# Kernel tuning notes

Hardware: AMD Instinct MI355X
Metric: run time of the kernel (lower is better)

Reference implementation:

```python
import jax, jax.numpy as jnp
import numpy as np

# Model dims
T0 = 2048      # tokens (batch*seq flattened)
D = 2048       # hidden_size
E = 256        # n_routed_experts
K = 8          # num_experts_per_tok
G = 8          # expert groups
EG = 32        # experts per group
R = 64         # tucker rank
I = 1408       # moe_intermediate_size


def setup_inputs() -> dict:
    key = jax.random.key(0)
    ks = jax.random.split(key, 12)
    f = lambda k, s: jax.random.normal(k, s, dtype=jnp.float32) * 0.02
    return {
        "hidden_states": jax.random.normal(ks[0], (T0, D), dtype=jnp.float32),
        "w_gate": f(ks[1], (D, E)),
        # Tucker factors per group: shared in-factor A, per-expert core C, shared out-factor B
        "A_gate": f(ks[2], (G, D, R)), "C_gate": f(ks[3], (G, EG, R, R)), "B_gate": f(ks[4], (G, R, I)),
        "A_up":   f(ks[5], (G, D, R)), "C_up":   f(ks[6], (G, EG, R, R)), "B_up":   f(ks[7], (G, R, I)),
        "A_down": f(ks[8], (G, I, R)), "C_down": f(ks[9], (G, EG, R, R)), "B_down": f(ks[10], (G, R, D)),
    }


def _tucker(x, A, C, B, inner):
    # x: [T, d_in], A: [d_in, R], C: [EG, R, R] gathered per-token, B: [R, d_out]
    h1 = x @ A                                    # [T, R]
    h2 = jnp.einsum('tr,trs->ts', h1, C[inner])   # per-token expert core
    return h2 @ B                                 # [T, d_out]


def reference(hidden_states, w_gate, A_gate, C_gate, B_gate,
              A_up, C_up, B_up, A_down, C_down, B_down):
    # Router: softmax in fp32, top-k, renormalize
    logits = hidden_states @ w_gate                              # [T0, E]
    probs = jax.nn.softmax(logits.astype(jnp.float32), axis=-1)
    rw, sel = jax.lax.top_k(probs, K)                            # [T0, K]
    rw = (rw / rw.sum(axis=-1, keepdims=True)).astype(hidden_states.dtype)

    idx = sel.reshape(-1)          # [T0*K] expert ids of dispatched rows
    gid = idx // EG                # group id
    inner = idx % EG               # expert within group
    x = jnp.repeat(hidden_states, K, axis=0)   # repeat_interleave dispatch [T0*K, D]

    out = jnp.zeros_like(x)
    for g in range(G):             # static loop over 8 structurally distinct groups
        m = (gid == g)[:, None]
        xg = jnp.where(m, x, 0.0)  # masked dispatch (zeros flow to zero through the MLP)
        go = _tucker(xg, A_gate[g], C_gate[g], B_gate[g], inner)
        uo = _tucker(xg, A_up[g],   C_up[g],   B_up[g],   inner)
        inter = jax.nn.silu(go) * uo
        do = _tucker(inter, A_down[g], C_down[g], B_down[g], inner)
        out = out + jnp.where(m, do, 0.0)

    # weighted combine
    return (out.reshape(T0, K, D) * rw[..., None]).sum(axis=1)
```

## Files before the change

### kernel.cpp

```cpp
#include <hip/hip_runtime.h>
#include <math.h>

constexpr int T0n = 2048;
constexpr int Dn  = 2048;
constexpr int En  = 256;
constexpr int Gn  = 8;
constexpr int EGn = 32;
constexpr int Rn  = 64;
constexpr int In  = 1408;

constexpr int NROWS = T0n * 8;
constexpr int SEGCAP = NROWS;
constexpr int KS_R = 4;
constexpr int NTILE_MAX = NROWS / 128 + Gn;
constexpr int CSPLIT = 8;

typedef __attribute__((ext_vector_type(8))) short s8v;
typedef __attribute__((ext_vector_type(4))) float f4v;
typedef __attribute__((ext_vector_type(4))) int i4v;
#define MFMA16(a, b, c) __builtin_amdgcn_mfma_f32_16x16x32_bf16(a, b, c, 0, 0, 0)
#define MFMAI8(a, b, c) __builtin_amdgcn_mfma_i32_16x16x64_i8(a, b, c, 0, 0, 0)

__device__ __forceinline__ unsigned short f2bf(float x) {
  unsigned int u = __float_as_uint(x);
  unsigned int r = (u + 0x7FFFu + ((u >> 16) & 1u)) >> 16;
  return (unsigned short)r;
}

struct TD { const float* src; unsigned short* dst; int rows, cols, nbx, per_batch, base; };
struct TD9 { TD t[9]; };

__global__ __launch_bounds__(256) void k_tcvt9(TD9 D) {
  __shared__ float tbuf[32][33];
  int id = blockIdx.x;
  int ti = 0;
#pragma unroll
  for (int i = 1; i < 9; ++i) ti = (id >= D.t[i].base) ? i : ti;
  TD d = D.t[ti];
  int local = id - d.base;
  int bz = local / d.per_batch;
  int rem = local - bz * d.per_batch;
  int by = rem / d.nbx;
  int bx = rem - by * d.nbx;

  size_t boff = (size_t)bz * d.rows * d.cols;
  const float* src = d.src + boff;
  unsigned short* dst = d.dst + boff;
  int c0 = bx * 32, r0 = by * 32;
  int tx = threadIdx.x & 31, ty = threadIdx.x >> 5;
  for (int i = ty; i < 32; i += 8)
    tbuf[i][tx] = src[(size_t)(r0 + i) * d.cols + c0 + tx];
  __syncthreads();
  for (int i = ty; i < 32; i += 8)
    dst[(size_t)(c0 + i) * d.rows + r0 + tx] = f2bf(tbuf[tx][i]);
}

__device__ __forceinline__ int4 limbs4(float v, double sc) {
  double d = (double)v * sc;
  d = fmin(fmax(d, -2.0e9), 2.0e9);
  int x = __double2int_rn(d);
  int l0 = (int)(signed char)(x & 0xff); x = (x - l0) >> 8;
  int l1 = (int)(signed char)(x & 0xff); x = (x - l1) >> 8;
  int l2 = (int)(signed char)(x & 0xff); x = (x - l2) >> 8;
  return make_int4(l0, l1, l2, x);
}

__global__ __launch_bounds__(256) void k_quant_h(
    const float* __restrict__ H, char* __restrict__ hq) {
  const size_t PL = (size_t)T0n * Dn;
  size_t i = (size_t)blockIdx.x * 256 + threadIdx.x;
  float4 v = *(const float4*)&H[i * 4];
  int4 a = limbs4(v.x, 268435456.0);
  int4 b = limbs4(v.y, 268435456.0);
  int4 c = limbs4(v.z, 268435456.0);
  int4 d = limbs4(v.w, 268435456.0);
  unsigned int p0 = (a.x & 0xff) | ((b.x & 0xff) << 8) | ((c.x & 0xff) << 16) | ((unsigned)(d.x & 0xff) << 24);
  unsigned int p1 = (a.y & 0xff) | ((b.y & 0xff) << 8) | ((c.y & 0xff) << 16) | ((unsigned)(d.y & 0xff) << 24);
  unsigned int p2 = (a.z & 0xff) | ((b.z & 0xff) << 8) | ((c.z & 0xff) << 16) | ((unsigned)(d.z & 0xff) << 24);
  unsigned int p3 = (a.w & 0xff) | ((b.w & 0xff) << 8) | ((c.w & 0xff) << 16) | ((unsigned)(d.w & 0xff) << 24);
  *(unsigned int*)&hq[0 * PL + i * 4] = p0;
  *(unsigned int*)&hq[1 * PL + i * 4] = p1;
  *(unsigned int*)&hq[2 * PL + i * 4] = p2;
  *(unsigned int*)&hq[3 * PL + i * 4] = p3;
}

__global__ __launch_bounds__(256) void k_quant_wT(
    const float* __restrict__ W, char* __restrict__ wqT) {
  __shared__ float tb[32][33];
  const size_t PL = (size_t)En * Dn;
  int kb = blockIdx.x * 32, nb = blockIdx.y * 32;
  int tx = threadIdx.x & 31, ty = threadIdx.x >> 5;
  for (int i = ty; i < 32; i += 8)
    tb[i][tx] = W[(size_t)(kb + i) * En + nb + tx];
  __syncthreads();
  for (int i = ty; i < 32; i += 8) {
    int4 l = limbs4(tb[tx][i], 8589934592.0);
    size_t off = (size_t)(nb + i) * Dn + kb + tx;
    wqT[0 * PL + off] = (char)l.x;
    wqT[1 * PL + off] = (char)l.y;
    wqT[2 * PL + off] = (char)l.z;
    wqT[3 * PL + off] = (char)l.w;
  }
}

__global__ __launch_bounds__(256) void k_router_i8(
    const char* __restrict__ hq, const char* __restrict__ wqT,
    float* __restrict__ part) {
  __shared__ __align__(16) char Asl[4][64][80];
  __shared__ __align__(16) char Bsl[4][64][80];
  const int n0 = blockIdx.x * 64, m0 = blockIdx.y * 64;
  const int kc = blockIdx.z;
  const int tid = threadIdx.x;
  const int w = tid >> 6, ln = tid & 63;
  const int quad = ln >> 4, lane16 = ln & 15;

  const char* ha = hq + ((size_t)w * T0n + m0 + ln) * Dn;
  const char* ba = wqT + ((size_t)w * En + n0 + ln) * Dn;

  i4v acc[4][5] = {};

  const int kbeg = kc * (Dn / KS_R);
  for (int k0 = kbeg; k0 < kbeg + Dn / KS_R; k0 += 64) {
#pragma unroll
    for (int q = 0; q < 4; ++q) {
      *(uint4*)&Asl[w][ln][q * 16] = *(const uint4*)&ha[k0 + q * 16];
      *(uint4*)&Bsl[w][ln][q * 16] = *(const uint4*)&ba[k0 + q * 16];
    }
    __syncthreads();
    i4v b0 = *(const i4v*)&Bsl[0][w * 16 + lane16][quad * 16];
    i4v b1 = *(const i4v*)&Bsl[1][w * 16 + lane16][quad * 16];
    i4v b2 = *(const i4v*)&Bsl[2][w * 16 + lane16][quad * 16];
    i4v b3 = *(const i4v*)&Bsl[3][w * 16 + lane16][quad * 16];
#pragma unroll
    for (int mt = 0; mt < 4; ++mt) {
      i4v a0 = *(const i4v*)&Asl[0][mt * 16 + lane16][quad * 16];
      i4v a1 = *(const i4v*)&Asl[1][mt * 16 + lane16][quad * 16];
      i4v a2 = *(const i4v*)&Asl[2][mt * 16 + lane16][quad * 16];
      i4v a3 = *(const i4v*)&Asl[3][mt * 16 + lane16][quad * 16];
      acc[mt][0] = MFMAI8(a0, b2, acc[mt][0]);
      acc[mt][0] = MFMAI8(a1, b1, acc[mt][0]);
      acc[mt][0] = MFMAI8(a2, b0, acc[mt][0]);
      acc[mt][1] = MFMAI8(a0, b3, acc[mt][1]);
      acc[mt][1] = MFMAI8(a1, b2, acc[mt][1]);
      acc[mt][1] = MFMAI8(a2, b1, acc[mt][1]);
      acc[mt][1] = MFMAI8(a3, b0, acc[mt][1]);
      acc[mt][2] = MFMAI8(a1, b3, acc[mt][2]);
      acc[mt][2] = MFMAI8(a2, b2, acc[mt][2]);
      acc[mt][2] = MFMAI8(a3, b1, acc[mt][2]);
      acc[mt][3] = MFMAI8(a2, b3, acc[mt][3]);
      acc[mt][3] = MFMAI8(a3, b2, acc[mt][3]);
      acc[mt][4] = MFMAI8(a3, b3, acc[mt][4]);
    }
    __syncthreads();
  }

  float* prow = part + (size_t)kc * T0n * En;
#pragma unroll
  for (int mt = 0; mt < 4; ++mt)
#pragma unroll
    for (int r = 0; r < 4; ++r) {
      int row = m0 + mt * 16 + quad * 4 + r;
      int col = n0 + w * 16 + lane16;
      double v = (double)acc[mt][0][r] * 0x1p-45 +
                 (double)acc[mt][1][r] * 0x1p-37 +
                 (double)acc[mt][2][r] * 0x1p-29 +
                 (double)acc[mt][3][r] * 0x1p-21 +
                 (double)acc[mt][4][r] * 0x1p-13;
      prow[(size_t)row * En + col] = (float)v;
    }
}

__global__ __launch_bounds__(256) void k_topk(
    const float* __restrict__ part, int* __restrict__ sel,
    float* __restrict__ rw, int* __restrict__ cnt_e) {
  const int wid = threadIdx.x >> 6, ln = threadIdx.x & 63;
  const int t = blockIdx.x * 4 + wid;

  double v[4];
#pragma unroll
  for (int j = 0; j < 4; ++j) {
    double s = 0.0;
#pragma unroll
    for (int kc = 0; kc < KS_R; ++kc)
      s += (double)part[((size_t)kc * T0n + t) * En + ln + 64 * j];
    v[j] = s;
  }

  float topv[8];
  int topi[8];
#pragma unroll
  for (int k = 0; k < 8; ++k) {
    double bv = v[0]; int bi = ln;
#pragma unroll
    for (int j = 1; j < 4; ++j) {
      int cand = ln + 64 * j;
      if (v[j] > bv || (v[j] == bv && cand < bi)) { bv = v[j]; bi = cand; }
    }
#pragma unroll
    for (int off = 32; off > 0; off >>= 1) {
      double ov = __shfl_xor(bv, off);
      int oi = __shfl_xor(bi, off);
      if (ov > bv || (ov == bv && oi < bi)) { bv = ov; bi = oi; }
    }
    topv[k] = (float)bv; topi[k] = bi;
    if ((bi & 63) == ln) v[bi >> 6] = -1e300;
  }

  if (ln < 8) {
    float m = topv[0];
    float ssum = 0.f;
#pragma unroll
    for (int k = 0; k < 8; ++k) ssum += expf(topv[k] - m);
    rw[t * 8 + ln] = expf(topv[ln] - m) / ssum;
    sel[t * 8 + ln] = topi[ln];
    atomicAdd(&cnt_e[topi[ln]], 1);
  }
}

__global__ __launch_bounds__(256) void k_scan(
    const int* __restrict__ cnt_e, int* __restrict__ off_e,
    int* __restrict__ cur_e, int* __restrict__ grp_n) {
  __shared__ int c[256];
  int tid = threadIdx.x;
  c[tid] = cnt_e[tid];
  __syncthreads();
  int g = tid >> 5, ei = tid & 31;
  int run = 0;
  for (int i = 0; i < ei; ++i) run += c[(g << 5) + i];
  off_e[tid] = g * SEGCAP + run;
  cur_e[tid] = g * SEGCAP + run;
  if (ei == 31) grp_n[g] = run + c[tid];
}

__global__ void k_scatter(const int* __restrict__ sel, int* __restrict__ cur_e,
                          int* __restrict__ rseg) {
  int i = blockIdx.x * 256 + threadIdx.x;
  int e = sel[i];
  int pos = atomicAdd(&cur_e[e], 1);
  rseg[pos] = i;
}

__global__ __launch_bounds__(512) void k_h1_mfma(
    const float* __restrict__ H,
    const unsigned short* __restrict__ AgT, const unsigned short* __restrict__ AuT,
    unsigned short* __restrict__ h1gb, unsigned short* __restrict__ h1ub) {
  const int t0 = blockIdx.x * 64;
  const int g = blockIdx.y;
  const unsigned short* Wg = AgT + (size_t)g * Rn * Dn;
  const unsigned short* Wu = AuT + (size_t)g * Rn * Dn;

  __shared__ unsigned short As[64 * 72];
  __shared__ unsigned short Bg_l[64 * 72];
  __shared__ unsigned short Bu_l[64 * 72];
  const int tid = threadIdx.x;
  const int w = tid >> 6, ln = tid & 63;
  const int path = w >> 2, ws = w & 3;
  const int quad = ln >> 4, lane16 = ln & 15;
  const int j = tid >> 3, q = (tid & 7) * 8;

  f4v S[4] = {};

  for (int k0 = 0; k0 < Dn; k0 += 64) {
    {
      float4 v0 = *(const float4*)&H[(size_t)(t0 + j) * Dn + k0 + q];
      float4 v1 = *(const float4*)&H[(size_t)(t0 + j) * Dn + k0 + q + 4];
      ushort4 o0, o1;
      o0.x = f2bf(v0.x); o0.y = f2bf(v0.y); o0.z = f2bf(v0.z); o0.w = f2bf(v0.w);
      o1.x = f2bf(v1.x); o1.y = f2bf(v1.y); o1.z = f2bf(v1.z); o1.w = f2bf(v1.w);
      *(ushort4*)&As[j * 72 + q] = o0;
      *(ushort4*)&As[j * 72 + q + 4] = o1;
      *(uint4*)&Bg_l[j * 72 + q] = *(const uint4*)&Wg[(size_t)j * Dn + k0 + q];
      *(uint4*)&Bu_l[j * 72 + q] = *(const uint4*)&Wu[(size_t)j * Dn + k0 + q];
    }
    __syncthreads();
    const unsigned short* Bl = path ? Bu_l : Bg_l;
#pragma unroll
    for (int kk = 0; kk < 2; ++kk) {
      s8v a = *(const s8v*)&As[(ws * 16 + lane16) * 72 + kk * 32 + quad * 8];
#pragma unroll
      for (int nt = 0; nt < 4; ++nt) {
        s8v b = *(const s8v*)&Bl[(nt * 16 + lane16) * 72 + kk * 32 + quad * 8];
        S[nt] = MFMA16(a, b, S[nt]);
      }
    }
    __syncthreads();
  }
  unsigned short* out = path ? h1ub : h1gb;
#pragma unroll
  for (int nt = 0; nt < 4; ++nt)
#pragma unroll
    for (int r = 0; r < 4; ++r) {
      int row = t0 + ws * 16 + quad * 4 + r;
      int col = g * 64 + nt * 16 + lane16;
      out[(size_t)row * (Gn * Rn) + col] = f2bf(S[nt][r]);
    }
}

__global__ __launch_bounds__(512) void k_core_gu(
    const unsigned short* __restrict__ h1gb, const unsigned short* __restrict__ h1ub,
    const unsigned short* __restrict__ CgT, const unsigned short* __restrict__ CuT,
    const int* __restrict__ rseg, const int* __restrict__ off_e,
    const int* __restrict__ cnt_e,
    unsigned short* __restrict__ h2gb, unsigned short* __restrict__ h2ub) {
  const int e = blockIdx.x;
  const int ne = cnt_e[e];
  if (ne == 0) return;
  const int g = e >> 5;
  const int base = off_e[e];
  __shared__ unsigned short Cg_l[64 * 72];
  __shared__ unsigned short Cu_l[64 * 72];
  __shared__ unsigned short Ags[64 * 72];
  __shared__ unsigned short Aus[64 * 72];
  __shared__ int rids[64];
  const int tid = threadIdx.x;
  const int w = tid >> 6, ln = tid & 63;
  const int path = w >> 2, ws = w & 3;
  const int quad = ln >> 4, lane16 = ln & 15;
  const int j = tid >> 3, q = (tid & 7) * 8;
  {
    const unsigned short* cg = CgT + (size_t)e * (Rn * Rn);
    const unsigned short* cu = CuT + (size_t)e * (Rn * Rn);
    *(uint4*)&Cg_l[j * 72 + q] = *(const uint4*)&cg[j * 64 + q];
    *(uint4*)&Cu_l[j * 72 + q] = *(const uint4*)&cu[j * 64 + q];
  }
  const int ntile = (ne + 63) >> 6;
  for (int it = 0; it < ntile; ++it) {
    int mi = it * 64 + j;
    int rid = (mi < ne) ? rseg[base + mi] : -1;
    if ((tid & 7) == 0) rids[j] = rid;
    uint4 zg = {0, 0, 0, 0}, zu = {0, 0, 0, 0};
    if (rid >= 0) {
      zg = *(const uint4*)&h1gb[(size_t)(rid >> 3) * (Gn * Rn) + g * 64 + q];
      zu = *(const uint4*)&h1ub[(size_t)(rid >> 3) * (Gn * Rn) + g * 64 + q];
    }
    *(uint4*)&Ags[j * 72 + q] = zg;
    *(uint4*)&Aus[j * 72 + q] = zu;
    __syncthreads();
    const unsigned short* Al = path ? Aus : Ags;
    const unsigned short* Cl = path ? Cu_l : Cg_l;
    f4v S[4] = {};
#pragma unroll
    for (int kk = 0; kk < 2; ++kk) {
      s8v a = *(const s8v*)&Al[(ws * 16 + lane16) * 72 + kk * 32 + quad * 8];
#pragma unroll
      for (int nt = 0; nt < 4; ++nt) {
        s8v b = *(const s8v*)&Cl[(nt * 16 + lane16) * 72 + kk * 32 + quad * 8];
        S[nt] = MFMA16(a, b, S[nt]);
      }
    }
    unsigned short* out = path ? h2ub : h2gb;
#pragma unroll
    for (int nt = 0; nt < 4; ++nt)
#pragma unroll
      for (int r = 0; r < 4; ++r) {
        int rid2 = rids[ws * 16 + quad * 4 + r];
        if (rid2 >= 0)
          out[(size_t)rid2 * 64 + nt * 16 + lane16] = f2bf(S[nt][r]);
      }
    __syncthreads();
  }
}

__global__ __launch_bounds__(256) void k_expand_mfma(
    const unsigned short* __restrict__ h2gb, const unsigned short* __restrict__ h2ub,
    const unsigned short* __restrict__ BgT, const unsigned short* __restrict__ BuT,
    const unsigned short* __restrict__ AdT,
    const int* __restrict__ rseg, const int* __restrict__ grp_n,
    float* __restrict__ h1d) {
  int t = blockIdx.x;
  int g = -1, m0 = 0, ng = 0;
  {
    int pre = 0;
#pragma unroll
    for (int gg = 0; gg < Gn; ++gg) {
      int n = grp_n[gg];
      int nt = (n + 127) >> 7;
      if (g < 0 && t < pre + nt) { g = gg; m0 = (t - pre) << 7; ng = n; }
      pre += nt;
    }
  }
  if (g < 0) return;
  const int c_beg = (blockIdx.y * 22) / CSPLIT;
  const int c_end = ((blockIdx.y + 1) * 22) / CSPLIT;

  __shared__ unsigned short Bg_l[64 * 72];
  __shared__ unsigned short Bu_l[64 * 72];
  __shared__ unsigned short Ad_l[64 * 72];
  __shared__ unsigned short inter_l[4][32 * 72];
  __shared__ int rids[128];

  const int tid = threadIdx.x;
  const int w = tid >> 6, ln = tid & 63;
  const int quad = ln >> 4, lane16 = ln & 15;

  if (tid < 128) rids[tid] = (m0 + tid < ng) ? rseg[g * SEGCAP + m0 + tid] : -1;
  __syncthreads();

  s8v ag[2][2], au[2][2];
#pragma unroll
  for (int mt = 0; mt < 2; ++mt) {
    int rid = rids[w * 32 + mt * 16 + lane16];
#pragma unroll
    for (int kk = 0; kk < 2; ++kk) {
      s8v zg = {}, zu = {};
      if (rid >= 0) {
        zg = *(const s8v*)&h2gb[(size_t)rid * 64 + kk * 32 + quad * 8];
        zu = *(const s8v*)&h2ub[(size_t)rid * 64 + kk * 32 + quad * 8];
      }
      ag[mt][kk] = zg;
      au[mt][kk] = zu;
    }
  }

  const unsigned short* Bg_base = BgT + (size_t)g * In * Rn;
  const unsigned short* Bu_base = BuT + (size_t)g * In * Rn;
  const unsigned short* Ad_base = AdT + (size_t)g * Rn * In;

  unsigned short* ib = &inter_l[w][0];
  f4v P[2][4] = {};

  for (int c = c_beg; c < c_end; ++c) {
    const int i0 = c * 64;
#pragma unroll
    for (int i = 0; i < 2; ++i) {
      int cq = tid + i * 256;
      int row = cq >> 3, co = (cq & 7) * 8;
      *(uint4*)&Bg_l[row * 72 + co] = *(const uint4*)&Bg_base[(size_t)(i0 + row) * Rn + co];
      *(uint4*)&Bu_l[row * 72 + co] = *(const uint4*)&Bu_base[(size_t)(i0 + row) * Rn + co];
      *(uint4*)&Ad_l[row * 72 + co] = *(const uint4*)&Ad_base[(size_t)row * In + i0 + co];
    }
    __syncthreads();

    f4v Sg[2][4] = {}, Su[2][4] = {};
#pragma unroll
    for (int kk = 0; kk < 2; ++kk) {
      s8v bg[4], bu[4];
#pragma unroll
      for (int nt = 0; nt < 4; ++nt) {
        bg[nt] = *(const s8v*)&Bg_l[(nt * 16 + lane16) * 72 + kk * 32 + quad * 8];
        bu[nt] = *(const s8v*)&Bu_l[(nt * 16 + lane16) * 72 + kk * 32 + quad * 8];
      }
#pragma unroll
      for (int mt = 0; mt < 2; ++mt)
#pragma unroll
        for (int nt = 0; nt < 4; ++nt) {
          Sg[mt][nt] = MFMA16(ag[mt][kk], bg[nt], Sg[mt][nt]);
          Su[mt][nt] = MFMA16(au[mt][kk], bu[nt], Su[mt][nt]);
        }
    }

#pragma unroll
    for (int mt = 0; mt < 2; ++mt)
#pragma unroll
      for (int nt = 0; nt < 4; ++nt)
#pragma unroll
        for (int r = 0; r < 4; ++r) {
          float sg = Sg[mt][nt][r];
          float v = sg / (1.f + __expf(-sg)) * Su[mt][nt][r];
          ib[(mt * 16 + quad * 4 + r) * 72 + nt * 16 + lane16] = f2bf(v);
        }
    asm volatile("s_waitcnt lgkmcnt(0)" ::: "memory");

#pragma unroll
    for (int kk = 0; kk < 2; ++kk) {
      s8v ai[2], bd[4];
#pragma unroll
      for (int mt = 0; mt < 2; ++mt)
        ai[mt] = *(const s8v*)&ib[(mt * 16 + lane16) * 72 + kk * 32 + quad * 8];
#pragma unroll
      for (int nt = 0; nt < 4; ++nt)
        bd[nt] = *(const s8v*)&Ad_l[(nt * 16 + lane16) * 72 + kk * 32 + quad * 8];
#pragma unroll
      for (int mt = 0; mt < 2; ++mt)
#pragma unroll
        for (int nt = 0; nt < 4; ++nt)
          P[mt][nt] = MFMA16(ai[mt], bd[nt], P[mt][nt]);
    }
    __syncthreads();
  }

#pragma unroll
  for (int mt = 0; mt < 2; ++mt)
#pragma unroll
    for (int nt = 0; nt < 4; ++nt)
#pragma unroll
      for (int r = 0; r < 4; ++r) {
        int lrow = w * 32 + mt * 16 + quad * 4 + r;
        int rid = rids[lrow];
        if (rid >= 0)
          atomicAdd(&h1d[(size_t)rid * 64 + nt * 16 + lane16], P[mt][nt][r]);
      }
}

__global__ __launch_bounds__(512) void k_core_down(
    const float* __restrict__ h1d, const unsigned short* __restrict__ CdT,
    const float* __restrict__ rw,
    const int* __restrict__ rseg, const int* __restrict__ off_e,
    const int* __restrict__ cnt_e,
    float* __restrict__ y) {
  const int e = blockIdx.x;
  const int ne = cnt_e[e];
  if (ne == 0) return;
  const int g = e >> 5;
  const int base = off_e[e];
  __shared__ unsigned short Bd_l[64 * 72];
  __shared__ unsigned short Ad_l[128 * 72];
  __shared__ int rids[128];
  const int tid = threadIdx.x;
  const int w = tid >> 6, ln = tid & 63;
  const int quad = ln >> 4, lane16 = ln & 15;
  {
    int j = tid >> 3, q = (tid & 7) * 8;
    const unsigned short* cd = CdT + (size_t)e * (Rn * Rn);
    *(uint4*)&Bd_l[j * 72 + q] = *(const uint4*)&cd[j * 64 + q];
  }
  const int gj = tid >> 2, gq = (tid & 3) * 16;
  const int ntile = (ne + 127) >> 7;
  for (int it = 0; it < ntile; ++it) {
    int mi = it * 128 + gj;
    int rid = (mi < ne) ? rseg[base + mi] : -1;
    if ((tid & 3) == 0) rids[gj] = rid;
#pragma unroll
    for (int i = 0; i < 4; ++i) {
      int kb = gq + i * 4;
      float4 vd = {0.f, 0.f, 0.f, 0.f};
      if (rid >= 0) vd = *(const float4*)&h1d[(size_t)rid * 64 + kb];
      ushort4 od;
      od.x = f2bf(vd.x); od.y = f2bf(vd.y); od.z = f2bf(vd.z); od.w = f2bf(vd.w);
      *(ushort4*)&Ad_l[gj * 72 + kb] = od;
    }
    __syncthreads();
    f4v Sd[4] = {};
#pragma unroll
    for (int kk = 0; kk < 2; ++kk) {
      s8v ad = *(const s8v*)&Ad_l[(w * 16 + lane16) * 72 + kk * 32 + quad * 8];
#pragma unroll
      for (int nt = 0; nt < 4; ++nt) {
        s8v bd = *(const s8v*)&Bd_l[(nt * 16 + lane16) * 72 + kk * 32 + quad * 8];
        Sd[nt] = MFMA16(ad, bd, Sd[nt]);
      }
    }
#pragma unroll
    for (int nt = 0; nt < 4; ++nt)
#pragma unroll
      for (int r = 0; r < 4; ++r) {
        int rid2 = rids[w * 16 + quad * 4 + r];
        if (rid2 >= 0) {
          float wgt = rw[rid2];
          atomicAdd(&y[(size_t)(rid2 >> 3) * (Gn * Rn) + g * 64 + nt * 16 + lane16],
                    wgt * Sd[nt][r]);
        }
      }
    __syncthreads();
  }
}

__global__ __launch_bounds__(256) void k_combine(
    const float* __restrict__ y, const unsigned short* __restrict__ BdT,
    float* __restrict__ outp) {
  const int t0 = blockIdx.y * 128, n0 = blockIdx.x * 128;
  __shared__ unsigned short As[128 * 72];
  __shared__ unsigned short Bs[128 * 72];
  const int tid = threadIdx.x;
  const int w = tid >> 6, ln = tid & 63;
  const int quad = ln >> 4, lane16 = ln & 15;
  const int mbase = (w >> 1) * 64, nbase = (w & 1) * 64;

  f4v acc[4][4] = {};

  for (int k0 = 0; k0 < Gn * Rn; k0 += 64) {
#pragma unroll
    for (int i = 0; i < 8; ++i) {
      int c = tid + i * 256;
      int row = c >> 4, cc = (c & 15) * 4;
      float4 v = *(const float4*)&y[(size_t)(t0 + row) * (Gn * Rn) + k0 + cc];
      ushort4 o;
      o.x = f2bf(v.x); o.y = f2bf(v.y); o.z = f2bf(v.z); o.w = f2bf(v.w);
      *(ushort4*)&As[row * 72 + cc] = o;
    }
#pragma unroll
    for (int i = 0; i < 4; ++i) {
      int c = tid + i * 256;
      int row = c >> 3, cc = (c & 7) * 8;
      *(uint4*)&Bs[row * 72 + cc] = *(const uint4*)&BdT[(size_t)(n0 + row) * (Gn * Rn) + k0 + cc];
    }
    __syncthreads();
#pragma unroll
    for (int kk = 0; kk < 2; ++kk) {
      s8v a[4], b[4];
#pragma unroll
      for (int mt = 0; mt < 4; ++mt)
        a[mt] = *(const s8v*)&As[(mbase + mt * 16 + lane16) * 72 + kk * 32 + quad * 8];
#pragma unroll
      for (int nt = 0; nt < 4; ++nt)
        b[nt] = *(const s8v*)&Bs[(nbase + nt * 16 + lane16) * 72 + kk * 32 + quad * 8];
#pragma unroll
      for (int mt = 0; mt < 4; ++mt)
#pragma unroll
        for (int nt = 0; nt < 4; ++nt)
          acc[mt][nt] = MFMA16(a[mt], b[nt], acc[mt][nt]);
    }
    __syncthreads();
  }
#pragma unroll
  for (int mt = 0; mt < 4; ++mt)
#pragma unroll
    for (int nt = 0; nt < 4; ++nt)
#pragma unroll
      for (int r = 0; r < 4; ++r)
        outp[(size_t)(t0 + mbase + mt * 16 + quad * 4 + r) * Dn +
             n0 + nbase + nt * 16 + lane16] = acc[mt][nt][r];
}

extern "C" void kernel_launch(void* const* d_in, const int* in_sizes, int n_in,
                              void* d_out, int out_size, void* d_ws, size_t ws_size,
                              hipStream_t stream) {
  const float* hidden = (const float*)d_in[0];
  const float* w_gate = (const float*)d_in[1];
  const float* A_gate = (const float*)d_in[2];
  const float* C_gate = (const float*)d_in[3];
  const float* B_gate = (const float*)d_in[4];
  const float* A_up   = (const float*)d_in[5];
  const float* C_up   = (const float*)d_in[6];
  const float* B_up   = (const float*)d_in[7];
  const float* A_down = (const float*)d_in[8];
  const float* C_down = (const float*)d_in[9];
  const float* B_down = (const float*)d_in[10];
  float* out = (float*)d_out;

  char* base = (char*)d_ws;
  size_t o = 0;
  unsigned short* h2gb = (unsigned short*)(base + o); o += (size_t)NROWS * Rn * 2;
  unsigned short* h2ub = (unsigned short*)(base + o); o += (size_t)NROWS * Rn * 2;
  unsigned short* AgT  = (unsigned short*)(base + o); o += (size_t)Gn * Rn * Dn * 2;
  unsigned short* AuT  = (unsigned short*)(base + o); o += (size_t)Gn * Rn * Dn * 2;
  unsigned short* BgT  = (unsigned short*)(base + o); o += (size_t)Gn * In * Rn * 2;
  unsigned short* BuT  = (unsigned short*)(base + o); o += (size_t)Gn * In * Rn * 2;
  unsigned short* AdT  = (unsigned short*)(base + o); o += (size_t)Gn * Rn * In * 2;
  unsigned short* BdT  = (unsigned short*)(base + o); o += (size_t)Dn * Gn * Rn * 2;
  unsigned short* CgT  = (unsigned short*)(base + o); o += (size_t)En * Rn * Rn * 2;
  unsigned short* CuT  = (unsigned short*)(base + o); o += (size_t)En * Rn * Rn * 2;
  unsigned short* CdT  = (unsigned short*)(base + o); o += (size_t)En * Rn * Rn * 2;
  unsigned short* h1gb = (unsigned short*)(base + o); o += (size_t)T0n * Gn * Rn * 2;
  unsigned short* h1ub = (unsigned short*)(base + o); o += (size_t)T0n * Gn * Rn * 2;
  float* h1d = (float*)(base + o); o += (size_t)NROWS * Rn * 4;
  float* y   = (float*)(base + o); o += (size_t)T0n * Gn * Rn * 4;
  float* rwp = (float*)(base + o); o += (size_t)NROWS * 4;
  int* sel   = (int*)(base + o); o += (size_t)NROWS * 4;
  int* rseg  = (int*)(base + o); o += (size_t)Gn * SEGCAP * 4;
  int* cnt_e = (int*)(base + o); o += En * 4;
  int* off_e = (int*)(base + o); o += En * 4;
  int* cur_e = (int*)(base + o); o += En * 4;
  int* grp_n = (int*)(base + o); o += Gn * 4;
  float* part = (float*)base;
  char* hq  = base + (size_t)KS_R * T0n * En * 4;
  char* wqT = hq + (size_t)4 * T0n * Dn;

  hipMemsetAsync(cnt_e, 0, En * sizeof(int), stream);

  k_quant_h<<<T0n * Dn / 1024, 256, 0, stream>>>(hidden, hq);
  k_quant_wT<<<dim3(Dn / 32, En / 32), 256, 0, stream>>>(w_gate, wqT);
  k_router_i8<<<dim3(En / 64, T0n / 64, KS_R), 256, 0, stream>>>(hq, wqT, part);
  k_topk<<<T0n / 4, 256, 0, stream>>>(part, sel, rwp, cnt_e);
  k_scan<<<1, 256, 0, stream>>>(cnt_e, off_e, cur_e, grp_n);
  k_scatter<<<NROWS / 256, 256, 0, stream>>>(sel, cur_e, rseg);

  hipMemsetAsync(h1d, 0, (size_t)NROWS * Rn * sizeof(float), stream);
  hipMemsetAsync(y,   0, (size_t)T0n * Gn * Rn * sizeof(float), stream);

  {
    TD9 D;
    D.t[0] = {A_gate, AgT, Dn, Rn, Rn / 32, (Rn / 32) * (Dn / 32), 0};
    D.t[1] = {A_up,   AuT, Dn, Rn, Rn / 32, (Rn / 32) * (Dn / 32), 1024};
    D.t[2] = {B_gate, BgT, Rn, In, In / 32, (In / 32) * (Rn / 32), 2048};
    D.t[3] = {B_up,   BuT, Rn, In, In / 32, (In / 32) * (Rn / 32), 2752};
    D.t[4] = {A_down, AdT, In, Rn, Rn / 32, (Rn / 32) * (In / 32), 3456};
    D.t[5] = {B_down, BdT, Gn * Rn, Dn, Dn / 32, (Dn / 32) * (Gn * Rn / 32), 4160};
    D.t[6] = {C_gate, CgT, Rn, Rn, 2, 4, 5184};
    D.t[7] = {C_up,   CuT, Rn, Rn, 2, 4, 6208};
    D.t[8] = {C_down, CdT, Rn, Rn, 2, 4, 7232};
    k_tcvt9<<<8256, 256, 0, stream>>>(D);
  }

  k_h1_mfma<<<dim3(T0n / 64, Gn), 512, 0, stream>>>(hidden, AgT, AuT, h1gb, h1ub);
  k_core_gu<<<En, 512, 0, stream>>>(h1gb, h1ub, CgT, CuT,
                                    rseg, off_e, cnt_e, h2gb, h2ub);
  k_expand_mfma<<<dim3(NTILE_MAX, CSPLIT), 256, 0, stream>>>(
      h2gb, h2ub, BgT, BuT, AdT, rseg, grp_n, h1d);
  k_core_down<<<En, 512, 0, stream>>>(h1d, CdT, rwp,
                                      rseg, off_e, cnt_e, y);
  k_combine<<<dim3(Dn / 128, T0n / 128), 256, 0, stream>>>(y, BdT, out);
}
```

Baseline: 319.0 us.

## Replace atomic split-K accumulation of h1d with per-split buffers summed in core_down

Expand-kernel split blocks now write their partial h1d results with plain stores into four separate scratch buffers instead of atomically adding into one buffer. The down-core kernel sums the four partials when it loads them. This removes the 4 MB memset and the global float atomics, and the split factor drops from 8 to 4 to match the buffer count. Three of the buffers alias scratch regions (AgT, CgT, h1gb) assumed dead by then. In exchange core_down reads four times the data, the expand launch has fewer blocks, and the aliasing depends on buffer sizes and ordering that are not fully visible.

```diff
diff --git a/kernel.cpp b/kernel.cpp
--- a/kernel.cpp
+++ b/kernel.cpp
@@ -13,7 +13,7 @@
 constexpr int SEGCAP = NROWS;
 constexpr int KS_R = 4;
 constexpr int NTILE_MAX = NROWS / 128 + Gn;
-constexpr int CSPLIT = 8;
+constexpr int CSPLIT = 4;
 
 typedef __attribute__((ext_vector_type(8))) short s8v;
 typedef __attribute__((ext_vector_type(4))) float f4v;
@@ -366,7 +366,8 @@
     const unsigned short* __restrict__ BgT, const unsigned short* __restrict__ BuT,
     const unsigned short* __restrict__ AdT,
     const int* __restrict__ rseg, const int* __restrict__ grp_n,
-    float* __restrict__ h1d) {
+    float* __restrict__ s0, float* __restrict__ s1,
+    float* __restrict__ s2, float* __restrict__ s3) {
   int t = blockIdx.x;
   int g = -1, m0 = 0, ng = 0;
   {
@@ -382,6 +383,8 @@
   if (g < 0) return;
   const int c_beg = (blockIdx.y * 22) / CSPLIT;
   const int c_end = ((blockIdx.y + 1) * 22) / CSPLIT;
+  float* hs = (blockIdx.y == 0) ? s0 : (blockIdx.y == 1) ? s1
+            : (blockIdx.y == 2) ? s2 : s3;
 
   __shared__ unsigned short Bg_l[64 * 72];
   __shared__ unsigned short Bu_l[64 * 72];
@@ -488,12 +491,14 @@
         int lrow = w * 32 + mt * 16 + quad * 4 + r;
         int rid = rids[lrow];
         if (rid >= 0)
-          atomicAdd(&h1d[(size_t)rid * 64 + nt * 16 + lane16], P[mt][nt][r]);
+          hs[(size_t)rid * 64 + nt * 16 + lane16] = P[mt][nt][r];
       }
 }
 
 __global__ __launch_bounds__(512) void k_core_down(
-    const float* __restrict__ h1d, const unsigned short* __restrict__ CdT,
+    const float* __restrict__ s0, const float* __restrict__ s1,
+    const float* __restrict__ s2, const float* __restrict__ s3,
+    const unsigned short* __restrict__ CdT,
     const float* __restrict__ rw,
     const int* __restrict__ rseg, const int* __restrict__ off_e,
     const int* __restrict__ cnt_e,
@@ -524,7 +529,17 @@
     for (int i = 0; i < 4; ++i) {
       int kb = gq + i * 4;
       float4 vd = {0.f, 0.f, 0.f, 0.f};
-      if (rid >= 0) vd = *(const float4*)&h1d[(size_t)rid * 64 + kb];
+      if (rid >= 0) {
+        size_t off = (size_t)rid * 64 + kb;
+        float4 a0 = *(const float4*)&s0[off];
+        float4 a1 = *(const float4*)&s1[off];
+        float4 a2 = *(const float4*)&s2[off];
+        float4 a3 = *(const float4*)&s3[off];
+        vd.x = (a0.x + a1.x) + (a2.x + a3.x);
+        vd.y = (a0.y + a1.y) + (a2.y + a3.y);
+        vd.z = (a0.z + a1.z) + (a2.z + a3.z);
+        vd.w = (a0.w + a1.w) + (a2.w + a3.w);
+      }
       ushort4 od;
       od.x = f2bf(vd.x); od.y = f2bf(vd.y); od.z = f2bf(vd.z); od.w = f2bf(vd.w);
       *(ushort4*)&Ad_l[gj * 72 + kb] = od;
@@ -655,6 +670,10 @@
   float* part = (float*)base;
   char* hq  = base + (size_t)KS_R * T0n * En * 4;
   char* wqT = hq + (size_t)4 * T0n * Dn;
+  float* h1s0 = h1d;
+  float* h1s1 = (float*)AgT;
+  float* h1s2 = (float*)CgT;
+  float* h1s3 = (float*)h1gb;
 
   hipMemsetAsync(cnt_e, 0, En * sizeof(int), stream);
 
@@ -665,8 +684,7 @@
   k_scan<<<1, 256, 0, stream>>>(cnt_e, off_e, cur_e, grp_n);
   k_scatter<<<NROWS / 256, 256, 0, stream>>>(sel, cur_e, rseg);
 
-  hipMemsetAsync(h1d, 0, (size_t)NROWS * Rn * sizeof(float), stream);
-  hipMemsetAsync(y,   0, (size_t)T0n * Gn * Rn * sizeof(float), stream);
+  hipMemsetAsync(y, 0, (size_t)T0n * Gn * Rn * sizeof(float), stream);
 
   {
     TD9 D;
@@ -686,8 +704,8 @@
   k_core_gu<<<En, 512, 0, stream>>>(h1gb, h1ub, CgT, CuT,
                                     rseg, off_e, cnt_e, h2gb, h2ub);
   k_expand_mfma<<<dim3(NTILE_MAX, CSPLIT), 256, 0, stream>>>(
-      h2gb, h2ub, BgT, BuT, AdT, rseg, grp_n, h1d);
-  k_core_down<<<En, 512, 0, stream>>>(h1d, CdT, rwp,
+      h2gb, h2ub, BgT, BuT, AdT, rseg, grp_n, h1s0, h1s1, h1s2, h1s3);
+  k_core_down<<<En, 512, 0, stream>>>(h1s0, h1s1, h1s2, h1s3, CdT, rwp,
                                       rseg, off_e, cnt_e, y);
   k_combine<<<dim3(Dn / 128, T0n / 128), 256, 0, stream>>>(y, BdT, out);
 }
```

Measured after the change: 324.8 us. About the same (+1.8%).
